# Performance work log

Measured on AMD Instinct MI355X. Metric: run time of the kernel, lower is better.

Reference implementation:

```python
import jax, jax.numpy as jnp
import numpy as np

FP8_MAX = 448.0  # e4m3 max, from scale = max(w) / (448.0 * 6.0) in the source


def setup_inputs() -> dict:
    key = jax.random.key(0)
    k_w, k_perm, k_x, k_b = jax.random.split(key, 4)
    T, K, O = 8192, 4096, 4096  # tokens = bsz*q_len, in_features, out_features

    # --- simulate init-time reorder_quantize_w ---
    w = jax.random.normal(k_w, (O, K), dtype=jnp.float32) * 0.02
    g_scale = jnp.max(jnp.abs(w)) / (FP8_MAX * 6.0)          # global weight scale
    perm = jax.random.permutation(k_perm, K)                  # outlier reorder index
    w_r = w[:, perm] / g_scale                                # reordered, globally scaled
    scale_w = jnp.max(jnp.abs(w_r), axis=1) / FP8_MAX         # per-out-channel scale (O,)
    W = jnp.round(w_r / scale_w[:, None])                     # quantized values (stored fp32)

    # --- simulate activation quantization (same reorder applied upstream) ---
    x = jax.random.normal(k_x, (T, K), dtype=jnp.float32)
    scale_x = (jnp.max(jnp.abs(x), axis=1, keepdims=True) / FP8_MAX)  # (T,1)
    qx = jnp.round(x / scale_x)                               # quantized values (stored fp32)

    bias = jax.random.normal(k_b, (O,), dtype=jnp.float32) * 0.01
    scale = jnp.asarray([g_scale], dtype=jnp.float32)         # fused global scale (x-global * w-global)

    return {"qx": qx, "W": W, "scale_x": scale_x, "scale_w": scale_w,
            "scale": scale, "bias": bias, "bsz": 4, "q_len": 2048}


def reference(qx, W, scale_x, scale_w, scale, bias, bsz, q_len):
    # agemm.matmul: low-bit GEMM with fused per-token (scale_x), per-channel (scale_w)
    # and global (scale) dequant scales.  y[t,o] = (sum_k qx[t,k]*W[o,k]) * sx[t] * sw[o] * s
    y = jnp.einsum('tk,ok->to', qx, W)           # (T, O) accumulate
    y = y * scale_x * scale_w[None, :] * scale[0]
    y = y + bias
    return y.reshape(bsz, q_len, -1)
```

## Files before the change

### kernel.cpp

```cpp
#include <hip/hip_runtime.h>

typedef __bf16 bf16_t;
typedef __bf16 bf16x8 __attribute__((ext_vector_type(8)));
typedef __bf16 bf16x4 __attribute__((ext_vector_type(4)));
typedef float f32x4 __attribute__((ext_vector_type(4)));

constexpr int TDIM = 8192;
constexpr int KDIM = 4096;
constexpr int ODIM = 4096;

__device__ __forceinline__ void async_ld16(void* lds, const void* g) {
    __builtin_amdgcn_global_load_lds(
        (const __attribute__((address_space(1))) unsigned int*)g,
        (__attribute__((address_space(3))) unsigned int*)lds,
        16, 0, 0);
}

__global__ __launch_bounds__(256) void cvt2_kernel(const float* __restrict__ a, bf16_t* __restrict__ da,
                                                   int nblk_a,
                                                   const float* __restrict__ w, bf16_t* __restrict__ dw) {
    int b = blockIdx.x;
    const float* src;
    bf16_t* dst;
    if (b < nblk_a) { src = a; dst = da; }
    else            { src = w; dst = dw; b -= nblk_a; }
    const size_t base = (size_t)b * 2048 + threadIdx.x * 4;
    const float4 v0 = *(const float4*)(src + base);
    const float4 v1 = *(const float4*)(src + base + 1024);
    bf16x4 o0, o1;
    o0[0] = (bf16_t)v0.x; o0[1] = (bf16_t)v0.y; o0[2] = (bf16_t)v0.z; o0[3] = (bf16_t)v0.w;
    o1[0] = (bf16_t)v1.x; o1[1] = (bf16_t)v1.y; o1[2] = (bf16_t)v1.z; o1[3] = (bf16_t)v1.w;
    *(bf16x4*)(dst + base) = o0;
    *(bf16x4*)(dst + base + 1024) = o1;
}

constexpr int BM = 256, BN = 256, BK = 64;
constexpr int NKT = KDIM / BK;
constexpr int NIT = NKT / 2;

#define BAR   __builtin_amdgcn_s_barrier()
#define SCB   __builtin_amdgcn_sched_barrier(0)
#define WLG   asm volatile("s_waitcnt lgkmcnt(0)" ::: "memory")
#define WV6   asm volatile("s_waitcnt vmcnt(6)" ::: "memory")
#define WV0   asm volatile("s_waitcnt vmcnt(0)" ::: "memory")
#define PRIO1 __builtin_amdgcn_s_setprio(1)
#define PRIO0 __builtin_amdgcn_s_setprio(0)

#define STG_A(c, kt, h) \
    async_ld16(lds_a + (c)*32768 + (h)*16384,        a_srcb + (size_t)((h)*128     )*KDIM + (kt)*64); \
    async_ld16(lds_a + (c)*32768 + (h)*16384 + 8192, a_srcb + (size_t)((h)*128 + 64)*KDIM + (kt)*64)
#define STG_B(c, kt, h) \
    async_ld16(lds_b + (c)*32768 + (h)*16384,        b_srcb + (size_t)((h)*128     )*KDIM + (kt)*64); \
    async_ld16(lds_b + (c)*32768 + (h)*16384 + 8192, b_srcb + (size_t)((h)*128 + 64)*KDIM + (kt)*64)

#define LD_A_LO(c) _Pragma("unroll") for (int m = 0; m < 4; ++m) { \
    af[m][0] = *(const bf16x8*)(a_rd + (c)*32768 + m*2048 + ck0); \
    af[m][1] = *(const bf16x8*)(a_rd + (c)*32768 + m*2048 + ck1); }
#define LD_A_HI(c) _Pragma("unroll") for (int m = 0; m < 4; ++m) { \
    af[m][0] = *(const bf16x8*)(a_rd + (c)*32768 + (m+4)*2048 + ck0); \
    af[m][1] = *(const bf16x8*)(a_rd + (c)*32768 + (m+4)*2048 + ck1); }
#define LD_B_ALL(c) _Pragma("unroll") for (int n = 0; n < 4; ++n) { \
    bfr[n][0] = *(const bf16x8*)(b_rd + (c)*32768 + n*2048 + ck0); \
    bfr[n][1] = *(const bf16x8*)(b_rd + (c)*32768 + n*2048 + ck1); }

#define MFMA16(MB, NB) \
  _Pragma("unroll") for (int m = 0; m < 4; ++m) \
  _Pragma("unroll") for (int n = 0; n < 2; ++n) \
  _Pragma("unroll") for (int k = 0; k < 2; ++k) \
    acc[(MB)+m][(NB)+n] = __builtin_amdgcn_mfma_f32_16x16x32_bf16( \
        af[m][k], bfr[(NB)+n][k], acc[(MB)+m][(NB)+n], 0, 0, 0)

__global__ __launch_bounds__(512, 2) void gemm8_kernel(
    const bf16_t* __restrict__ A, const bf16_t* __restrict__ B,
    const float* __restrict__ scale_x, const float* __restrict__ scale_w,
    const float* __restrict__ gscale, const float* __restrict__ bias,
    float* __restrict__ out)
{
    __shared__ __attribute__((aligned(16))) char smem[131072];

    const int tid = threadIdx.x;
    const int lin = (blockIdx.x & 7) * 64 + (blockIdx.x >> 3);
    const int row0 = (lin >> 4) * BM;
    const int col0 = (lin & 15) * BN;

    const int ld_row = tid >> 3;
    const int ld_ch  = (tid & 7) ^ (ld_row & 7);
    const bf16_t* a_srcb = A + (size_t)(row0 + ld_row) * KDIM + ld_ch * 8;
    const bf16_t* b_srcb = B + (size_t)(col0 + ld_row) * KDIM + ld_ch * 8;
    char* lds_a = smem + tid * 16;
    char* lds_b = smem + 65536 + tid * 16;

    const int lane = tid & 63;
    const int wid  = tid >> 6;
    const int wm   = wid >> 2;
    const int wn   = wid & 3;
    const int fr   = lane & 15;
    const int q    = lane >> 4;
    const int swz  = lane & 7;
    const int ck0  = ((q ^ swz)) * 16;
    const int ck1  = (((4 | q) ^ swz)) * 16;
    const char* a_rd = smem + (wm * 128 + fr) * 128;
    const char* b_rd = smem + 65536 + (wn * 64 + fr) * 128;

    f32x4 acc[8][4] = {};
    bf16x8 af[4][2], bfr[4][2];

    STG_B(0, 0, 0); STG_B(0, 0, 1);
    STG_A(0, 0, 0); STG_A(0, 0, 1);
    STG_B(1, 1, 0); STG_B(1, 1, 1);
    STG_A(1, 1, 0);
    WV6; SCB; BAR; SCB;

#pragma unroll 1
    for (int i = 0; i < NIT; ++i) {
        const int tp = 2 * i + 2;
        const bool pf = (tp < NKT);
        LD_A_LO(0); LD_B_ALL(0);
        STG_A(1, 2 * i + 1, 1);
        BAR; WLG; SCB;
        PRIO1; MFMA16(0, 0); PRIO0; SCB; BAR; SCB;
        if (pf) { STG_B(0, tp, 0); }
        BAR; SCB;
        PRIO1; MFMA16(0, 2); PRIO0; SCB; BAR; SCB;
        LD_A_HI(0);
        if (pf) { STG_B(0, tp, 1); }
        BAR; WLG; SCB;
        PRIO1; MFMA16(4, 0); PRIO0; SCB; BAR; SCB;
        if (pf) { STG_A(0, tp, 0); }
        BAR; SCB;
        PRIO1; MFMA16(4, 2); PRIO0; SCB;
        if (i + 1 < NIT) { WV6; } else { WV0; }
        SCB; BAR; SCB;
        LD_A_LO(1); LD_B_ALL(1);
        if (pf) { STG_A(0, tp, 1); }
        BAR; WLG; SCB;
        PRIO1; MFMA16(0, 0); PRIO0; SCB; BAR; SCB;
        if (pf) { STG_B(1, tp + 1, 0); }
        BAR; SCB;
        PRIO1; MFMA16(0, 2); PRIO0; SCB; BAR; SCB;
        LD_A_HI(1);
        if (pf) { STG_B(1, tp + 1, 1); }
        BAR; WLG; SCB;
        PRIO1; MFMA16(4, 0); PRIO0; SCB; BAR; SCB;
        if (pf) { STG_A(1, tp + 1, 0); }
        BAR; SCB;
        PRIO1; MFMA16(4, 2); PRIO0; SCB;
        WV6; SCB; BAR; SCB;
    }

    const float gs = gscale[0];
    const int trow = row0 + wm * 128 + q * 4;
    const int ocol = col0 + wn * 64 + fr;
#pragma unroll
    for (int nt = 0; nt < 4; ++nt) {
        const int o = ocol + nt * 16;
        const float sws = scale_w[o] * gs;
        const float bv = bias[o];
#pragma unroll
        for (int mt = 0; mt < 8; ++mt) {
#pragma unroll
            for (int ii = 0; ii < 4; ++ii) {
                const int t = trow + mt * 16 + ii;
                out[(size_t)t * ODIM + o] = acc[mt][nt][ii] * (scale_x[t] * sws) + bv;
            }
        }
    }
}

constexpr int FBM = 128, FBN = 128, FBK = 32;

__global__ __launch_bounds__(256, 4) void gemm_fallback(
    const float* __restrict__ Afp, const float* __restrict__ Bfp,
    const float* __restrict__ scale_x, const float* __restrict__ scale_w,
    const float* __restrict__ gscale, const float* __restrict__ bias,
    float* __restrict__ out) {
    __shared__ bf16_t sA[FBM * FBK];
    __shared__ bf16_t sB[FBN * FBK];

    const int tid = threadIdx.x;
    const int bn = blockIdx.x & 31;
    const int bm = blockIdx.x >> 5;
    const int row0 = bm * FBM;
    const int col0 = bn * FBN;

    const int lane = tid & 63;
    const int wid = tid >> 6;
    const int wm = (wid >> 1) * 64;
    const int wn = (wid & 1) * 64;
    const int fr = lane & 15;
    const int q  = lane >> 4;
    const int s_fr = (fr >> 1) & 3;
    const int kc = ((q ^ s_fr) * 8);

    f32x4 acc[4][4] = {};

    for (int k0 = 0; k0 < KDIM; k0 += FBK) {
        const int r = tid >> 2;
        const int cg2 = (tid & 3) ^ ((tid >> 3) & 3);
#pragma unroll
        for (int h = 0; h < 2; ++h) {
            const int rr = r + h * 64;
            const float4 va0 = *(const float4*)(Afp + (size_t)(row0 + rr) * KDIM + k0 + cg2 * 8);
            const float4 va1 = *(const float4*)(Afp + (size_t)(row0 + rr) * KDIM + k0 + cg2 * 8 + 4);
            const float4 vb0 = *(const float4*)(Bfp + (size_t)(col0 + rr) * KDIM + k0 + cg2 * 8);
            const float4 vb1 = *(const float4*)(Bfp + (size_t)(col0 + rr) * KDIM + k0 + cg2 * 8 + 4);
            bf16x8 pa, pb;
            pa[0] = (bf16_t)va0.x; pa[1] = (bf16_t)va0.y; pa[2] = (bf16_t)va0.z; pa[3] = (bf16_t)va0.w;
            pa[4] = (bf16_t)va1.x; pa[5] = (bf16_t)va1.y; pa[6] = (bf16_t)va1.z; pa[7] = (bf16_t)va1.w;
            pb[0] = (bf16_t)vb0.x; pb[1] = (bf16_t)vb0.y; pb[2] = (bf16_t)vb0.z; pb[3] = (bf16_t)vb0.w;
            pb[4] = (bf16_t)vb1.x; pb[5] = (bf16_t)vb1.y; pb[6] = (bf16_t)vb1.z; pb[7] = (bf16_t)vb1.w;
            *(bf16x8*)&sA[rr * FBK + (tid & 3) * 8] = pa;
            *(bf16x8*)&sB[rr * FBK + (tid & 3) * 8] = pb;
        }
        __syncthreads();

        bf16x8 a8[4], b8[4];
#pragma unroll
        for (int mt = 0; mt < 4; ++mt)
            a8[mt] = *(const bf16x8*)&sA[(wm + mt * 16 + fr) * FBK + kc];
#pragma unroll
        for (int nt = 0; nt < 4; ++nt)
            b8[nt] = *(const bf16x8*)&sB[(wn + nt * 16 + fr) * FBK + kc];
#pragma unroll
        for (int mt = 0; mt < 4; ++mt)
#pragma unroll
            for (int nt = 0; nt < 4; ++nt)
                acc[mt][nt] = __builtin_amdgcn_mfma_f32_16x16x32_bf16(a8[mt], b8[nt], acc[mt][nt], 0, 0, 0);
        __syncthreads();
    }

    const float gs = gscale[0];
    const int rbase = q * 4;
#pragma unroll
    for (int nt = 0; nt < 4; ++nt) {
        const int o = col0 + wn + nt * 16 + fr;
        const float swv = scale_w[o] * gs;
        const float bv = bias[o];
#pragma unroll
        for (int mt = 0; mt < 4; ++mt) {
#pragma unroll
            for (int i = 0; i < 4; ++i) {
                const int t = row0 + wm + mt * 16 + rbase + i;
                out[(size_t)t * ODIM + o] = acc[mt][nt][i] * (scale_x[t] * swv) + bv;
            }
        }
    }
}

extern "C" void kernel_launch(void* const* d_in, const int* in_sizes, int n_in,
                              void* d_out, int out_size, void* d_ws, size_t ws_size,
                              hipStream_t stream) {
    const float* qx   = (const float*)d_in[0];
    const float* W    = (const float*)d_in[1];
    const float* sx   = (const float*)d_in[2];
    const float* sw   = (const float*)d_in[3];
    const float* gs   = (const float*)d_in[4];
    const float* bias = (const float*)d_in[5];
    float* out = (float*)d_out;

    const size_t nA = (size_t)TDIM * KDIM;
    const size_t nW = (size_t)ODIM * KDIM;

    if (ws_size >= (nA + nW) * sizeof(bf16_t)) {
        bf16_t* Abf = (bf16_t*)d_ws;
        bf16_t* Wbf = Abf + nA;
        const int nblk_a = (int)(nA / 2048);
        const int nblk_w = (int)(nW / 2048);
        cvt2_kernel<<<dim3(nblk_a + nblk_w), dim3(256), 0, stream>>>(qx, Abf, nblk_a, W, Wbf);
        gemm8_kernel<<<dim3((TDIM / BM) * (ODIM / BN)), dim3(512), 0, stream>>>(
            Abf, Wbf, sx, sw, gs, bias, out);
    } else {
        gemm_fallback<<<dim3((TDIM / FBM) * (ODIM / FBN)), dim3(256), 0, stream>>>(
            qx, W, sx, sw, gs, bias, out);
    }
}
```

Baseline: 493.9 us.

## Split B fragment loads and software-pipeline LDS reads behind MFMA phases

The B fragment LDS reads are split into two halves. Each half is now issued right after the preceding MFMA cluster, so LDS reads for the next phase overlap the current math instead of sitting at the head of each half-iteration. The vmcnt waits move earlier, and the first tile's A/B fragments are preloaded before the loop, with the last iteration guarded. This reduces exposed LDS latency between MFMA bursts, at the cost of tighter barrier/wait ordering that could introduce hazards or extra stalls.

After: 487.5 us. About the same (-1.3%).

```diff
diff --git a/kernel.cpp b/kernel.cpp
--- a/kernel.cpp
+++ b/kernel.cpp
@@ -59,7 +59,10 @@
 #define LD_A_HI(c) _Pragma("unroll") for (int m = 0; m < 4; ++m) { \
     af[m][0] = *(const bf16x8*)(a_rd + (c)*32768 + (m+4)*2048 + ck0); \
     af[m][1] = *(const bf16x8*)(a_rd + (c)*32768 + (m+4)*2048 + ck1); }
-#define LD_B_ALL(c) _Pragma("unroll") for (int n = 0; n < 4; ++n) { \
+#define LD_B01(c) _Pragma("unroll") for (int n = 0; n < 2; ++n) { \
+    bfr[n][0] = *(const bf16x8*)(b_rd + (c)*32768 + n*2048 + ck0); \
+    bfr[n][1] = *(const bf16x8*)(b_rd + (c)*32768 + n*2048 + ck1); }
+#define LD_B23(c) _Pragma("unroll") for (int n = 2; n < 4; ++n) { \
     bfr[n][0] = *(const bf16x8*)(b_rd + (c)*32768 + n*2048 + ck0); \
     bfr[n][1] = *(const bf16x8*)(b_rd + (c)*32768 + n*2048 + ck1); }
 
@@ -110,42 +113,45 @@
     STG_B(1, 1, 0); STG_B(1, 1, 1);
     STG_A(1, 1, 0);
     WV6; SCB; BAR; SCB;
+    LD_A_LO(0); LD_B01(0); SCB;
 
 #pragma unroll 1
     for (int i = 0; i < NIT; ++i) {
         const int tp = 2 * i + 2;
         const bool pf = (tp < NKT);
-        LD_A_LO(0); LD_B_ALL(0);
+        const bool last = (i + 1 == NIT);
         STG_A(1, 2 * i + 1, 1);
         BAR; WLG; SCB;
-        PRIO1; MFMA16(0, 0); PRIO0; SCB; BAR; SCB;
+        PRIO1; MFMA16(0, 0); PRIO0; SCB;
+        LD_B23(0); SCB; BAR; SCB;
         if (pf) { STG_B(0, tp, 0); }
-        BAR; SCB;
-        PRIO1; MFMA16(0, 2); PRIO0; SCB; BAR; SCB;
-        LD_A_HI(0);
+        BAR; WLG; SCB;
+        PRIO1; MFMA16(0, 2); PRIO0; SCB;
+        LD_A_HI(0); SCB; BAR; SCB;
         if (pf) { STG_B(0, tp, 1); }
         BAR; WLG; SCB;
         PRIO1; MFMA16(4, 0); PRIO0; SCB; BAR; SCB;
         if (pf) { STG_A(0, tp, 0); }
-        BAR; SCB;
+        if (!last) { WV6; } else { WV0; }
+        SCB; BAR; SCB;
         PRIO1; MFMA16(4, 2); PRIO0; SCB;
-        if (i + 1 < NIT) { WV6; } else { WV0; }
-        SCB; BAR; SCB;
-        LD_A_LO(1); LD_B_ALL(1);
+        LD_A_LO(1); LD_B01(1); SCB; BAR; SCB;
         if (pf) { STG_A(0, tp, 1); }
         BAR; WLG; SCB;
-        PRIO1; MFMA16(0, 0); PRIO0; SCB; BAR; SCB;
+        PRIO1; MFMA16(0, 0); PRIO0; SCB;
+        LD_B23(1); SCB; BAR; SCB;
         if (pf) { STG_B(1, tp + 1, 0); }
-        BAR; SCB;
-        PRIO1; MFMA16(0, 2); PRIO0; SCB; BAR; SCB;
-        LD_A_HI(1);
+        BAR; WLG; SCB;
+        PRIO1; MFMA16(0, 2); PRIO0; SCB;
+        LD_A_HI(1); SCB; BAR; SCB;
         if (pf) { STG_B(1, tp + 1, 1); }
         BAR; WLG; SCB;
         PRIO1; MFMA16(4, 0); PRIO0; SCB; BAR; SCB;
         if (pf) { STG_A(1, tp + 1, 0); }
-        BAR; SCB;
+        WV6; SCB; BAR; SCB;
         PRIO1; MFMA16(4, 2); PRIO0; SCB;
-        WV6; SCB; BAR; SCB;
+        if (!last) { LD_A_LO(0); LD_B01(0); }
+        SCB; BAR; SCB;
     }
 
     const float gs = gscale[0];
```
